# Optimization experiments

Hardware: AMD Instinct MI355X
Metric: run time of the kernel (lower is better)

The kernel has to match this reference:

```python
import jax, jax.numpy as jnp
import numpy as np

B, N, K, DIM = 8, 2048, 8, 128
EPS = 1e-5  # BatchNorm eps (torch default); BN evaluated in inference mode with running stats


def _xavier(key, o, i):
    lim = float(np.sqrt(6.0 / (i + o)))
    return jax.random.uniform(key, (o, i), jnp.float32, -lim, lim)


def setup_inputs() -> dict:
    key = jax.random.key(0)
    ks = jax.random.split(key, 8)
    x = jax.random.normal(ks[0], (B, 3, N), jnp.float32)
    w0 = _xavier(ks[1], DIM, 3)
    b0 = jnp.zeros((DIM,), jnp.float32)
    ws = jnp.stack([_xavier(ks[2 + i], DIM, DIM) for i in range(2)])  # [2,DIM,DIM]
    bs = jnp.zeros((2, DIM), jnp.float32)
    # BatchNorm (eval-mode) params / running stats, mildly randomized so math is exercised
    bn_g = 1.0 + 0.1 * jax.random.normal(ks[4], (3, DIM), jnp.float32)
    bn_b = 0.1 * jax.random.normal(ks[5], (3, DIM), jnp.float32)
    bn_m = 0.1 * jax.random.normal(ks[6], (3, DIM), jnp.float32)
    bn_v = jax.random.uniform(ks[7], (3, DIM), jnp.float32, 0.5, 1.5)
    return {"x": x, "w0": w0, "b0": b0, "ws": ws, "bs": bs,
            "bn_g": bn_g, "bn_b": bn_b, "bn_m": bn_m, "bn_v": bn_v}


def _group(x):
    # x: [B,3,N] -> relative kNN coords [B,3,N,K] (torch code uses [B,3,K,N]; axis order
    # is immaterial since the MLP is pointwise and the max is over the neighbor axis)
    inner = jnp.einsum('bcn,bcm->bnm', x, x)
    sq = jnp.sum(x * x, axis=1)                      # [B,N]
    dist = sq[:, :, None] - 2.0 * inner + sq[:, None, :]
    idx = jax.lax.top_k(-dist, K)[1]                 # [B,N,K] nearest (incl. self)
    grouped = jax.vmap(lambda xi, ii: xi[:, ii])(x, idx)  # [B,3,N,K]
    return grouped - x[:, :, :, None]


def _block(h, w, b, g, be, m, v):
    # 1x1 conv + eval-mode BatchNorm + ReLU over channel axis 1
    h = jnp.einsum('oc,bcnk->bonk', w, h) + b[None, :, None, None]
    scale = (g / jnp.sqrt(v + EPS))[None, :, None, None]
    h = (h - m[None, :, None, None]) * scale + be[None, :, None, None]
    return jax.nn.relu(h)


def reference(x, w0, b0, ws, bs, bn_g, bn_b, bn_m, bn_v):
    h = _group(x)                                    # [B,3,N,K]
    h = _block(h, w0, b0, bn_g[0], bn_b[0], bn_m[0], bn_v[0])
    for i in range(2):
        h = _block(h, ws[i], bs[i], bn_g[i + 1], bn_b[i + 1], bn_m[i + 1], bn_v[i + 1])
    return jnp.max(h, axis=3)                        # [B,DIM,N]
```

## Files before the change

kernel.cpp:

```cpp
#include <hip/hip_runtime.h>


#define EPSF 1e-5f
#define FMAXV 3.402823466e+38f

#define NB 8
#define NN 2048
#define KNBR 8
#define DIMF 128
#define NQ (NB * NN)
#define NPAIR (NQ * KNBR)

#define OFF16_W1H 0
#define OFF16_W1L 16384
#define OFF16_W2H 32768
#define OFF16_W2L 49152
#define OFF_C1 32896
#define OFF_C2 33024
#define OFF_W0F 33152
#define OFF_IDX 33792

typedef __attribute__((ext_vector_type(4))) float f32x4;
typedef __attribute__((ext_vector_type(8))) short short8v;

__device__ __forceinline__ float relu_f(float a) { return fmaxf(a, 0.0f); }

__device__ __forceinline__ void split3(float f, unsigned& hi, unsigned& lo) {
  const unsigned u = __float_as_uint(f);
  const unsigned h = (u + 0x7FFFu + ((u >> 16) & 1u)) >> 16;
  const float hf = __uint_as_float(h << 16);
  lo = __float_as_uint(f - hf) >> 16;
  hi = h;
}

__device__ __forceinline__ f32x4 mfma16x16x32bf(short8v a, short8v b, f32x4 c) {
  return __builtin_amdgcn_mfma_f32_16x16x32_bf16(a, b, c, 0, 0, 0);
}

#define KCSWAP(a, b)                  \
  {                                   \
    const float mn_ = fminf(a, b);    \
    const float mx_ = fmaxf(a, b);    \
    (a) = mn_; (b) = mx_;             \
  }

#define SORT8(d0, d1, d2, d3, d4, d5, d6, d7)                   \
  KCSWAP(d0, d1) KCSWAP(d2, d3) KCSWAP(d4, d5) KCSWAP(d6, d7)   \
  KCSWAP(d0, d2) KCSWAP(d1, d3) KCSWAP(d4, d6) KCSWAP(d5, d7)   \
  KCSWAP(d1, d2) KCSWAP(d5, d6)                                 \
  KCSWAP(d0, d4) KCSWAP(d1, d5) KCSWAP(d2, d6) KCSWAP(d3, d7)   \
  KCSWAP(d2, d4) KCSWAP(d3, d5)                                 \
  KCSWAP(d1, d2) KCSWAP(d3, d4) KCSWAP(d5, d6)

#define KCLEAN8()                                               \
  KCSWAP(k0, k4) KCSWAP(k1, k5) KCSWAP(k2, k6) KCSWAP(k3, k7)   \
  KCSWAP(k0, k2) KCSWAP(k1, k3) KCSWAP(k4, k6) KCSWAP(k5, k7)   \
  KCSWAP(k0, k1) KCSWAP(k2, k3) KCSWAP(k4, k5) KCSWAP(k6, k7)

#define KFOLD8(d0, d1, d2, d3, d4, d5, d6, d7)                  \
  {                                                             \
    k0 = fminf(k0, d7); k1 = fminf(k1, d6);                     \
    k2 = fminf(k2, d5); k3 = fminf(k3, d4);                     \
    k4 = fminf(k4, d3); k5 = fminf(k5, d2);                     \
    k6 = fminf(k6, d1); k7 = fminf(k7, d0);                     \
    KCLEAN8()                                                   \
  }

#define KMERGE(mv)                                              \
  {                                                             \
    const float q0_ = __shfl_xor(k0, mv, 64);                   \
    const float q1_ = __shfl_xor(k1, mv, 64);                   \
    const float q2_ = __shfl_xor(k2, mv, 64);                   \
    const float q3_ = __shfl_xor(k3, mv, 64);                   \
    const float q4_ = __shfl_xor(k4, mv, 64);                   \
    const float q5_ = __shfl_xor(k5, mv, 64);                   \
    const float q6_ = __shfl_xor(k6, mv, 64);                   \
    const float q7_ = __shfl_xor(k7, mv, 64);                   \
    k0 = fminf(k0, q7_); k1 = fminf(k1, q6_);                   \
    k2 = fminf(k2, q5_); k3 = fminf(k3, q4_);                   \
    k4 = fminf(k4, q3_); k5 = fminf(k5, q2_);                   \
    k6 = fminf(k6, q1_); k7 = fminf(k7, q0_);                   \
    KCLEAN8()                                                   \
  }

__global__ __launch_bounds__(512, 4) void knn_kernel(
    const float* __restrict__ x, const float* __restrict__ w0,
    const float* __restrict__ b0, const float* __restrict__ wstk,
    const float* __restrict__ bstk, const float* __restrict__ g,
    const float* __restrict__ be, const float* __restrict__ bm,
    const float* __restrict__ bv, float* __restrict__ ws) {
  __shared__ float2 xyp[2080];
  __shared__ float2 zsp[2080];
  const int t = threadIdx.x;
  const int bid = blockIdx.x;

  if (bid >= 1024) {
    const int i = (bid - 1024) * 512 + t;
    unsigned short* __restrict__ wsh = (unsigned short*)ws;
    const int fo = i >> 7, k = i & 127;
    const float s1 = g[128 + fo] / sqrtf(bv[128 + fo] + EPSF);
    const float s2 = g[256 + fo] / sqrtf(bv[256 + fo] + EPSF);
    unsigned h1, l1, h2, l2;
    split3(wstk[i] * s1, h1, l1);
    split3(wstk[16384 + i] * s2, h2, l2);
    const int dst = ((fo >> 4) * 4 + (k >> 5)) * 512 +
                    (((k >> 3) & 3) * 16 + (fo & 15)) * 8 + (k & 7);
    wsh[OFF16_W1H + dst] = (unsigned short)h1;
    wsh[OFF16_W1L + dst] = (unsigned short)l1;
    wsh[OFF16_W2H + dst] = (unsigned short)h2;
    wsh[OFF16_W2L + dst] = (unsigned short)l2;
    if (bid == 1024 && t < 128) {
      const int f = t;
      const float s0 = g[f] / sqrtf(bv[f] + EPSF);
      const float s1b = g[128 + f] / sqrtf(bv[128 + f] + EPSF);
      const float s2b = g[256 + f] / sqrtf(bv[256 + f] + EPSF);
      ws[OFF_C1 + f] = (bstk[f] - bm[128 + f]) * s1b + be[128 + f];
      ws[OFF_C2 + f] = (bstk[128 + f] - bm[256 + f]) * s2b + be[256 + f];
      float4 wv;
      wv.x = w0[3 * f + 0] * s0;
      wv.y = w0[3 * f + 1] * s0;
      wv.z = w0[3 * f + 2] * s0;
      wv.w = (b0[f] - bm[f]) * s0 + be[f];
      *((float4*)(ws + OFF_W0F) + f) = wv;
    }
    return;
  }

  const int bb = bid >> 7;
  const int qloc0 = (bid & 127) * 16;
  const float* __restrict__ xb = x + bb * 3 * NN;

#pragma unroll
  for (int k = 0; k < 4; ++k) {
    const int i = t + k * 512;
    const float a0 = xb[i];
    const float a1 = xb[2048 + i];
    const float a2 = xb[4096 + i];
    const float sq = fmaf(a2, a2, fmaf(a1, a1, a0 * a0));
    const int ii = i + (i >> 6);
    xyp[ii] = make_float2(a0, a1);
    zsp[ii] = make_float2(a2, sq);
  }

  const int qi = t >> 5;
  const int sg = t & 31;
  const int n = qloc0 + qi;
  const int q = bb * NN + n;
  const float qx0 = xb[n], qx1 = xb[2048 + n], qx2 = xb[4096 + n];
  const float sqn = fmaf(qx2, qx2, fmaf(qx1, qx1, qx0 * qx0));
  __syncthreads();

  const float2* __restrict__ xr = xyp + sg * 65;
  const float2* __restrict__ zr = zsp + sg * 65;

  float dv[64];
  float k0 = FMAXV, k1 = FMAXV, k2 = FMAXV, k3 = FMAXV,
        k4 = FMAXV, k5 = FMAXV, k6 = FMAXV, k7 = FMAXV;
#pragma unroll
  for (int bt = 0; bt < 8; ++bt) {
    float d0, d1, d2, d3, d4, d5, d6, d7;
#define KD(j, dj)                                                        \
    {                                                                    \
      const float2 cxy = xr[bt * 8 + (j)];                               \
      const float2 czs = zr[bt * 8 + (j)];                               \
      const float inner =                                                \
          fmaf(qx2, czs.x, fmaf(qx1, cxy.y, qx0 * cxy.x));               \
      dj = (sqn - 2.0f * inner) + czs.y;                                 \
    }
    KD(0, d0) KD(1, d1) KD(2, d2) KD(3, d3)
    KD(4, d4) KD(5, d5) KD(6, d6) KD(7, d7)
#undef KD
    dv[bt * 8 + 0] = d0; dv[bt * 8 + 1] = d1;
    dv[bt * 8 + 2] = d2; dv[bt * 8 + 3] = d3;
    dv[bt * 8 + 4] = d4; dv[bt * 8 + 5] = d5;
    dv[bt * 8 + 6] = d6; dv[bt * 8 + 7] = d7;
    SORT8(d0, d1, d2, d3, d4, d5, d6, d7)
    KFOLD8(d0, d1, d2, d3, d4, d5, d6, d7)
  }

  KMERGE(1) KMERGE(2) KMERGE(4) KMERGE(8) KMERGE(16)
  const float thr = k7;

  unsigned am = 0, bm2 = 0;
#pragma unroll
  for (int mm = 0; mm < 32; ++mm) am |= (dv[mm] <= thr) ? (1u << mm) : 0u;
#pragma unroll
  for (int mm = 0; mm < 32; ++mm)
    bm2 |= (dv[32 + mm] <= thr) ? (1u << mm) : 0u;

  const int cnt = __popc(am) + __popc(bm2);
  int inc = cnt, tq;
  tq = __shfl_up(inc, 1, 32); inc += (sg >= 1) ? tq : 0;
  tq = __shfl_up(inc, 2, 32); inc += (sg >= 2) ? tq : 0;
  tq = __shfl_up(inc, 4, 32); inc += (sg >= 4) ? tq : 0;
  tq = __shfl_up(inc, 8, 32); inc += (sg >= 8) ? tq : 0;
  tq = __shfl_up(inc, 16, 32); inc += (sg >= 16) ? tq : 0;
  int pos = inc - cnt;

  int* __restrict__ idxg = (int*)(ws + OFF_IDX);
  {
    unsigned w = am;
    while (w) {
      const int b = __ffs(w) - 1;
      w &= w - 1;
      if (pos < 8) idxg[q * 8 + pos] = bb * NN + sg * 64 + b;
      ++pos;
    }
    w = bm2;
    while (w) {
      const int b = __ffs(w) - 1;
      w &= w - 1;
      if (pos < 8) idxg[q * 8 + pos] = bb * NN + sg * 64 + 32 + b;
      ++pos;
    }
  }
}

__global__ __launch_bounds__(256, 2) void fused_kernel(
    const float* __restrict__ x, float* __restrict__ ws,
    float* __restrict__ out) {
  extern __shared__ char smem[];
  unsigned* __restrict__ H = (unsigned*)(smem + 32768);
  float* __restrict__ OS = (float*)(smem + 49152);
  float4* __restrict__ W0L = (float4*)(smem + 65536);

  const int* __restrict__ idxg = (const int*)(ws + OFF_IDX);
  const unsigned short* __restrict__ wsu = (const unsigned short*)ws;

  const int t = threadIdx.x;
  const int lane = t & 63, w = t >> 6;
  const int wc = w;
  const int bid = blockIdx.x;
  const int bb = bid & 7, qseg = bid >> 3;
  const int chunk0 = bb * 512 + qseg * 8;
  const float* __restrict__ xb = x + bb * 3 * NN;

  if (t < 128) {
    const float4 wv = *((const float4*)(ws + OFF_W0F) + t);
    W0L[((t & 7) << 4) | (t >> 3)] = wv;
  }

  short8v w1h[2][4], w1l[2][4], w2h[2][4], w2l[2][4];
#pragma unroll
  for (int ft = 0; ft < 2; ++ft)
#pragma unroll
    for (int ks = 0; ks < 4; ++ks) {
      const int off = ((wc * 2 + ft) * 4 + ks) * 512 + lane * 8;
      w1h[ft][ks] = *(const short8v*)(wsu + OFF16_W1H + off);
      w1l[ft][ks] = *(const short8v*)(wsu + OFF16_W1L + off);
      w2h[ft][ks] = *(const short8v*)(wsu + OFF16_W2H + off);
      w2l[ft][ks] = *(const short8v*)(wsu + OFF16_W2L + off);
    }

  const float c1v0 = (ws + OFF_C1)[wc * 32 + (lane & 15)];
  const float c1v1 = (ws + OFF_C1)[wc * 32 + 16 + (lane & 15)];
  const float c2v0 = (ws + OFF_C2)[wc * 32 + (lane & 15)];
  const float c2v1 = (ws + OFF_C2)[wc * 32 + 16 + (lane & 15)];

  const int row = t >> 3, part8 = t & 7;
  __syncthreads();

#define PACK_WRITE_A(base, hv, kc)                              \
  {                                                             \
    unsigned hh[8], ll[8];                                      \
    _Pragma("unroll") for (int e = 0; e < 8; ++e)               \
        split3(hv[e], hh[e], ll[e]);                            \
    int4 hp, lp;                                                \
    hp.x = (int)(hh[0] | (hh[1] << 16));                        \
    hp.y = (int)(hh[2] | (hh[3] << 16));                        \
    hp.z = (int)(hh[4] | (hh[5] << 16));                        \
    hp.w = (int)(hh[6] | (hh[7] << 16));                        \
    lp.x = (int)(ll[0] | (ll[1] << 16));                        \
    lp.y = (int)(ll[2] | (ll[3] << 16));                        \
    lp.z = (int)(ll[4] | (ll[5] << 16));                        \
    lp.w = (int)(ll[6] | (ll[7] << 16));                        \
    const int col = (kc) ^ (row & 7);                           \
    *(int4*)((base) + row * 256 + col * 16) = hp;               \
    *(int4*)((base) + 8192 + row * 256 + col * 16) = lp;        \
  }

#define STAGE_A(base, R0, R1, R2)                               \
  {                                                             \
    float hv0[8], hv1[8];                                       \
    _Pragma("unroll") for (int e = 0; e < 8; ++e) {             \
      const float4 wa = W0L[e * 16 + part8 * 2];                \
      const float4 wb = W0L[e * 16 + part8 * 2 + 1];            \
      hv0[e] = relu_f(                                          \
          fmaf(wa.z, R2, fmaf(wa.y, R1, fmaf(wa.x, R0, wa.w))));\
      hv1[e] = relu_f(                                          \
          fmaf(wb.z, R2, fmaf(wb.y, R1, fmaf(wb.x, R0, wb.w))));\
    }                                                           \
    PACK_WRITE_A(base, hv0, part8 * 2)                          \
    PACK_WRITE_A(base, hv1, part8 * 2 + 1)                      \
  }

  {
    const int gp = chunk0 * 32 + row;
    const int mg = idxg[gp];
    const int mloc = mg & 2047, nloc = (gp >> 3) & 2047;
    const float r0 = xb[mloc] - xb[nloc];
    const float r1 = xb[2048 + mloc] - xb[2048 + nloc];
    const float r2 = xb[4096 + mloc] - xb[4096 + nloc];
    STAGE_A(smem, r0, r1, r2)
  }
  __syncthreads();

#pragma unroll 1
  for (int j = 0; j < 8; ++j) {
    char* __restrict__ Acur = smem + (j & 1) * 16384;
    char* __restrict__ Anxt = smem + ((j & 1) ^ 1) * 16384;

    int mg_next = 0, gp_next = 0;
    if (j < 7) {
      gp_next = (chunk0 + j + 1) * 32 + row;
      mg_next = idxg[gp_next];
    }

    f32x4 acc[2][2];
#pragma unroll
    for (int pt = 0; pt < 2; ++pt)
#pragma unroll
      for (int ft = 0; ft < 2; ++ft) acc[pt][ft] = (f32x4){0.f, 0.f, 0.f, 0.f};
    __builtin_amdgcn_s_setprio(1);
#pragma unroll
    for (int ks = 0; ks < 4; ++ks) {
      const int kc = ks * 4 + (lane >> 4);
#pragma unroll
      for (int pt = 0; pt < 2; ++pt) {
        const int arow = pt * 16 + (lane & 15);
        const int col = kc ^ (arow & 7);
        const short8v ah = *(const short8v*)(Acur + arow * 256 + col * 16);
        const short8v al =
            *(const short8v*)(Acur + 8192 + arow * 256 + col * 16);
#pragma unroll
        for (int ft = 0; ft < 2; ++ft) {
          acc[pt][ft] = mfma16x16x32bf(al, w1h[ft][ks], acc[pt][ft]);
          acc[pt][ft] = mfma16x16x32bf(ah, w1l[ft][ks], acc[pt][ft]);
          acc[pt][ft] = mfma16x16x32bf(ah, w1h[ft][ks], acc[pt][ft]);
        }
      }
    }
    __builtin_amdgcn_s_setprio(0);

    float r0n = 0.f, r1n = 0.f, r2n = 0.f;
    if (j < 7) {
      const int mloc = mg_next & 2047, nloc = (gp_next >> 3) & 2047;
      r0n = xb[mloc] - xb[nloc];
      r1n = xb[2048 + mloc] - xb[2048 + nloc];
      r2n = xb[4096 + mloc] - xb[4096 + nloc];
    }

#pragma unroll
    for (int pt = 0; pt < 2; ++pt)
#pragma unroll
      for (int ft = 0; ft < 2; ++ft) {
        const int fo = wc * 32 + ft * 16 + (lane & 15);
        const int cc = fo >> 2;
        const float cb = ft ? c1v1 : c1v0;
#pragma unroll
        for (int reg = 0; reg < 4; ++reg) {
          const int p = pt * 16 + (lane >> 4) * 4 + reg;
          const float vv = relu_f(acc[pt][ft][reg] + cb);
          unsigned hh, ll;
          split3(vv, hh, ll);
          H[p * 128 + ((cc ^ (p & 7)) << 2) + (fo & 3)] = (hh << 16) | ll;
        }
      }
    __syncthreads();

    f32x4 acc2[2][2];
#pragma unroll
    for (int pt = 0; pt < 2; ++pt)
#pragma unroll
      for (int ft = 0; ft < 2; ++ft) acc2[pt][ft] = (f32x4){0.f, 0.f, 0.f, 0.f};
    __builtin_amdgcn_s_setprio(1);
#pragma unroll
    for (int ks = 0; ks < 4; ++ks) {
      const int cc0 = ks * 8 + (lane >> 4) * 2;
#pragma unroll
      for (int pt = 0; pt < 2; ++pt) {
        const int p = pt * 16 + (lane & 15);
        const int4 u0 = *(const int4*)&H[p * 128 + ((cc0 ^ (p & 7)) << 2)];
        const int4 u1 = *(const int4*)&H[p * 128 + (((cc0 + 1) ^ (p & 7)) << 2)];
        const unsigned uu[8] = {(unsigned)u0.x, (unsigned)u0.y, (unsigned)u0.z,
                                (unsigned)u0.w, (unsigned)u1.x, (unsigned)u1.y,
                                (unsigned)u1.z, (unsigned)u1.w};
        short8v ah, al;
#pragma unroll
        for (int e = 0; e < 8; ++e) {
          ah[e] = (short)(uu[e] >> 16);
          al[e] = (short)(uu[e] & 0xFFFFu);
        }
#pragma unroll
        for (int ft = 0; ft < 2; ++ft) {
          acc2[pt][ft] = mfma16x16x32bf(al, w2h[ft][ks], acc2[pt][ft]);
          acc2[pt][ft] = mfma16x16x32bf(ah, w2l[ft][ks], acc2[pt][ft]);
          acc2[pt][ft] = mfma16x16x32bf(ah, w2h[ft][ks], acc2[pt][ft]);
        }
      }
    }
    __builtin_amdgcn_s_setprio(0);
    __syncthreads();

    {
      const int g = lane >> 4;
#pragma unroll
      for (int pt = 0; pt < 2; ++pt)
#pragma unroll
        for (int ft = 0; ft < 2; ++ft) {
          const int fo = wc * 32 + ft * 16 + (lane & 15);
          const float cb = ft ? c2v1 : c2v0;
          const float v0 = relu_f(acc2[pt][ft][0] + cb);
          const float v1 = relu_f(acc2[pt][ft][1] + cb);
          const float v2 = relu_f(acc2[pt][ft][2] + cb);
          const float v3 = relu_f(acc2[pt][ft][3] + cb);
          float m = fmaxf(fmaxf(v0, v1), fmaxf(v2, v3));
          m = fmaxf(m, __shfl_xor(m, 16, 64));
          if ((g & 1) == 0) {
            const int qloc = pt * 2 + (g >> 1);
            OS[(j * 4 + qloc) * 128 + fo] = m;
          }
        }
    }

    if (j < 7) {
      STAGE_A(Anxt, r0n, r1n, r2n)
    }
    __syncthreads();
  }

  {
    const int f = t >> 1, seg = t & 1;
    float* __restrict__ op =
        out + (long)(bb * 128 + f) * 2048 + qseg * 32 + seg * 16;
#pragma unroll
    for (int u = 0; u < 4; ++u) {
      float4 o;
      o.x = OS[(seg * 16 + u * 4 + 0) * 128 + f];
      o.y = OS[(seg * 16 + u * 4 + 1) * 128 + f];
      o.z = OS[(seg * 16 + u * 4 + 2) * 128 + f];
      o.w = OS[(seg * 16 + u * 4 + 3) * 128 + f];
      *(float4*)(op + u * 4) = o;
    }
  }
}

extern "C" void kernel_launch(void* const* d_in, const int* in_sizes, int n_in,
                              void* d_out, int out_size, void* d_ws,
                              size_t ws_size, hipStream_t stream) {
  (void)in_sizes; (void)n_in; (void)out_size; (void)ws_size;
  const float* x = (const float*)d_in[0];
  const float* w0 = (const float*)d_in[1];
  const float* b0 = (const float*)d_in[2];
  const float* wst = (const float*)d_in[3];
  const float* bst = (const float*)d_in[4];
  const float* g = (const float*)d_in[5];
  const float* be = (const float*)d_in[6];
  const float* bm = (const float*)d_in[7];
  const float* bv = (const float*)d_in[8];
  float* out = (float*)d_out;
  float* ws = (float*)d_ws;

  hipFuncSetAttribute((const void*)fused_kernel,
                      hipFuncAttributeMaxDynamicSharedMemorySize, 69632);

  knn_kernel<<<1056, 512, 0, stream>>>(x, w0, b0, wst, bst, g, be, bm, bv, ws);
  fused_kernel<<<512, 256, 67584, stream>>>(x, ws, out);
}
```

Before: 60.90 us.

## Software-pipeline layer-1 and layer-2 GEMMs with double-buffered hidden tile

Restructures the fused MLP loop so the layer-2 GEMM of chunk j runs in the same phase as the layer-1 GEMM of chunk j+1, using a double-buffered hidden-activation tile in LDS. This cuts one block-wide barrier per iteration and lets the two MFMA streams interleave. The per-block output staging buffer is halved and flushed in two parts, and dynamic LDS grows, which could limit how many blocks fit per CU.

Result: faster. 59.28 us (median of 2 runs) (-2.7%).

```diff
diff --git a/kernel.cpp b/kernel.cpp
--- a/kernel.cpp
+++ b/kernel.cpp
@@ -220,9 +220,8 @@
     const float* __restrict__ x, float* __restrict__ ws,
     float* __restrict__ out) {
   extern __shared__ char smem[];
-  unsigned* __restrict__ H = (unsigned*)(smem + 32768);
-  float* __restrict__ OS = (float*)(smem + 49152);
-  float4* __restrict__ W0L = (float4*)(smem + 65536);
+  float* __restrict__ OS = (float*)(smem + 65536);
+  float4* __restrict__ W0L = (float4*)(smem + 73728);
 
   const int* __restrict__ idxg = (const int*)(ws + OFF_IDX);
   const unsigned short* __restrict__ wsu = (const unsigned short*)ws;
@@ -294,155 +293,159 @@
     PACK_WRITE_A(base, hv1, part8 * 2 + 1)                      \
   }
 
+#define G1_TO_H(Abase, Hbase)                                           \
+  {                                                                     \
+    f32x4 acc[2][2];                                                    \
+    _Pragma("unroll") for (int pt = 0; pt < 2; ++pt)                    \
+        _Pragma("unroll") for (int ft = 0; ft < 2; ++ft)                \
+            acc[pt][ft] = (f32x4){0.f, 0.f, 0.f, 0.f};                  \
+    __builtin_amdgcn_s_setprio(1);                                      \
+    _Pragma("unroll") for (int ks = 0; ks < 4; ++ks) {                  \
+      const int kc = ks * 4 + (lane >> 4);                              \
+      _Pragma("unroll") for (int pt = 0; pt < 2; ++pt) {                \
+        const int arow = pt * 16 + (lane & 15);                         \
+        const int col = kc ^ (arow & 7);                                \
+        const short8v ah =                                              \
+            *(const short8v*)((Abase) + arow * 256 + col * 16);         \
+        const short8v al =                                              \
+            *(const short8v*)((Abase) + 8192 + arow * 256 + col * 16);  \
+        _Pragma("unroll") for (int ft = 0; ft < 2; ++ft) {              \
+          acc[pt][ft] = mfma16x16x32bf(al, w1h[ft][ks], acc[pt][ft]);   \
+          acc[pt][ft] = mfma16x16x32bf(ah, w1l[ft][ks], acc[pt][ft]);   \
+          acc[pt][ft] = mfma16x16x32bf(ah, w1h[ft][ks], acc[pt][ft]);   \
+        }                                                               \
+      }                                                                 \
+    }                                                                   \
+    __builtin_amdgcn_s_setprio(0);                                      \
+    unsigned* __restrict__ Hp = (unsigned*)(Hbase);                     \
+    _Pragma("unroll") for (int pt = 0; pt < 2; ++pt)                    \
+        _Pragma("unroll") for (int ft = 0; ft < 2; ++ft) {              \
+      const int fo = wc * 32 + ft * 16 + (lane & 15);                   \
+      const int cc = fo >> 2;                                           \
+      const float cb = ft ? c1v1 : c1v0;                                \
+      _Pragma("unroll") for (int reg = 0; reg < 4; ++reg) {             \
+        const int p = pt * 16 + (lane >> 4) * 4 + reg;                  \
+        const float vv = relu_f(acc[pt][ft][reg] + cb);                 \
+        unsigned hh, ll;                                                \
+        split3(vv, hh, ll);                                             \
+        Hp[p * 128 + ((cc ^ (p & 7)) << 2) + (fo & 3)] = (hh << 16) | ll; \
+      }                                                                 \
+    }                                                                   \
+  }
+
+#define G2_TO_OS(Hbase, CH)                                             \
+  {                                                                     \
+    const unsigned* __restrict__ Hp = (const unsigned*)(Hbase);         \
+    f32x4 acc2[2][2];                                                   \
+    _Pragma("unroll") for (int pt = 0; pt < 2; ++pt)                    \
+        _Pragma("unroll") for (int ft = 0; ft < 2; ++ft)                \
+            acc2[pt][ft] = (f32x4){0.f, 0.f, 0.f, 0.f};                 \
+    __builtin_amdgcn_s_setprio(1);                                      \
+    _Pragma("unroll") for (int ks = 0; ks < 4; ++ks) {                  \
+      const int cc0 = ks * 8 + (lane >> 4) * 2;                         \
+      _Pragma("unroll") for (int pt = 0; pt < 2; ++pt) {                \
+        const int p = pt * 16 + (lane & 15);                            \
+        const int4 u0 = *(const int4*)&Hp[p * 128 + ((cc0 ^ (p & 7)) << 2)]; \
+        const int4 u1 =                                                 \
+            *(const int4*)&Hp[p * 128 + (((cc0 + 1) ^ (p & 7)) << 2)];  \
+        const unsigned uu[8] = {(unsigned)u0.x, (unsigned)u0.y,         \
+                                (unsigned)u0.z, (unsigned)u0.w,         \
+                                (unsigned)u1.x, (unsigned)u1.y,         \
+                                (unsigned)u1.z, (unsigned)u1.w};        \
+        short8v ah, al;                                                 \
+        _Pragma("unroll") for (int e = 0; e < 8; ++e) {                 \
+          ah[e] = (short)(uu[e] >> 16);                                 \
+          al[e] = (short)(uu[e] & 0xFFFFu);                             \
+        }                                                               \
+        _Pragma("unroll") for (int ft = 0; ft < 2; ++ft) {              \
+          acc2[pt][ft] = mfma16x16x32bf(al, w2h[ft][ks], acc2[pt][ft]); \
+          acc2[pt][ft] = mfma16x16x32bf(ah, w2l[ft][ks], acc2[pt][ft]); \
+          acc2[pt][ft] = mfma16x16x32bf(ah, w2h[ft][ks], acc2[pt][ft]); \
+        }                                                               \
+      }                                                                 \
+    }                                                                   \
+    __builtin_amdgcn_s_setprio(0);                                      \
+    const int g = lane >> 4;                                            \
+    _Pragma("unroll") for (int pt = 0; pt < 2; ++pt)                    \
+        _Pragma("unroll") for (int ft = 0; ft < 2; ++ft) {              \
+      const int fo = wc * 32 + ft * 16 + (lane & 15);                   \
+      const float cb = ft ? c2v1 : c2v0;                                \
+      const float v0 = relu_f(acc2[pt][ft][0] + cb);                    \
+      const float v1 = relu_f(acc2[pt][ft][1] + cb);                    \
+      const float v2 = relu_f(acc2[pt][ft][2] + cb);                    \
+      const float v3 = relu_f(acc2[pt][ft][3] + cb);                    \
+      float m = fmaxf(fmaxf(v0, v1), fmaxf(v2, v3));                    \
+      m = fmaxf(m, __shfl_xor(m, 16, 64));                              \
+      if ((g & 1) == 0) {                                               \
+        const int qloc = pt * 2 + (g >> 1);                             \
+        OS[(((CH) & 3) * 4 + qloc) * 128 + fo] = m;                     \
+      }                                                                 \
+    }                                                                   \
+  }
+
+#define OS_FLUSH(h)                                                     \
+  {                                                                     \
+    const int f = t >> 1, sh = t & 1;                                   \
+    float* __restrict__ op = out + (long)(bb * 128 + f) * 2048 +        \
+                             qseg * 32 + (h) * 16 + sh * 8;             \
+    float4 o1, o2;                                                      \
+    o1.x = OS[(sh * 8 + 0) * 128 + f];                                  \
+    o1.y = OS[(sh * 8 + 1) * 128 + f];                                  \
+    o1.z = OS[(sh * 8 + 2) * 128 + f];                                  \
+    o1.w = OS[(sh * 8 + 3) * 128 + f];                                  \
+    o2.x = OS[(sh * 8 + 4) * 128 + f];                                  \
+    o2.y = OS[(sh * 8 + 5) * 128 + f];                                  \
+    o2.z = OS[(sh * 8 + 6) * 128 + f];                                  \
+    o2.w = OS[(sh * 8 + 7) * 128 + f];                                  \
+    *(float4*)op = o1;                                                  \
+    *(float4*)(op + 4) = o2;                                            \
+  }
+
+#define LOAD_R(CH, MG, R0, R1, R2)                     \
+  {                                                    \
+    const int mloc = (MG) & 2047;                      \
+    const int nloc = ((((CH) * 32 + row)) >> 3) & 2047;\
+    R0 = xb[mloc] - xb[nloc];                          \
+    R1 = xb[2048 + mloc] - xb[2048 + nloc];            \
+    R2 = xb[4096 + mloc] - xb[4096 + nloc];            \
+  }
+
   {
-    const int gp = chunk0 * 32 + row;
-    const int mg = idxg[gp];
-    const int mloc = mg & 2047, nloc = (gp >> 3) & 2047;
-    const float r0 = xb[mloc] - xb[nloc];
-    const float r1 = xb[2048 + mloc] - xb[2048 + nloc];
-    const float r2 = xb[4096 + mloc] - xb[4096 + nloc];
+    const int mg0 = idxg[(chunk0 + 0) * 32 + row];
+    const int mg1 = idxg[(chunk0 + 1) * 32 + row];
+    float r0, r1, r2;
+    LOAD_R(chunk0 + 0, mg0, r0, r1, r2)
     STAGE_A(smem, r0, r1, r2)
-  }
-  __syncthreads();
+    __syncthreads();
+    G1_TO_H(smem, smem + 32768)
+    LOAD_R(chunk0 + 1, mg1, r0, r1, r2)
+    STAGE_A(smem + 16384, r0, r1, r2)
+    __syncthreads();
+  }
 
 #pragma unroll 1
   for (int j = 0; j < 8; ++j) {
-    char* __restrict__ Acur = smem + (j & 1) * 16384;
-    char* __restrict__ Anxt = smem + ((j & 1) ^ 1) * 16384;
-
-    int mg_next = 0, gp_next = 0;
+    int mg2 = 0;
+    if (j < 6) mg2 = idxg[(chunk0 + j + 2) * 32 + row];
+
+    G2_TO_OS(smem + 32768 + (j & 1) * 16384, j)
+
     if (j < 7) {
-      gp_next = (chunk0 + j + 1) * 32 + row;
-      mg_next = idxg[gp_next];
-    }
-
-    f32x4 acc[2][2];
-#pragma unroll
-    for (int pt = 0; pt < 2; ++pt)
-#pragma unroll
-      for (int ft = 0; ft < 2; ++ft) acc[pt][ft] = (f32x4){0.f, 0.f, 0.f, 0.f};
-    __builtin_amdgcn_s_setprio(1);
-#pragma unroll
-    for (int ks = 0; ks < 4; ++ks) {
-      const int kc = ks * 4 + (lane >> 4);
-#pragma unroll
-      for (int pt = 0; pt < 2; ++pt) {
-        const int arow = pt * 16 + (lane & 15);
-        const int col = kc ^ (arow & 7);
-        const short8v ah = *(const short8v*)(Acur + arow * 256 + col * 16);
-        const short8v al =
-            *(const short8v*)(Acur + 8192 + arow * 256 + col * 16);
-#pragma unroll
-        for (int ft = 0; ft < 2; ++ft) {
-          acc[pt][ft] = mfma16x16x32bf(al, w1h[ft][ks], acc[pt][ft]);
-          acc[pt][ft] = mfma16x16x32bf(ah, w1l[ft][ks], acc[pt][ft]);
-          acc[pt][ft] = mfma16x16x32bf(ah, w1h[ft][ks], acc[pt][ft]);
-        }
+      G1_TO_H(smem + ((j + 1) & 1) * 16384,
+              smem + 32768 + ((j + 1) & 1) * 16384)
+      if (j < 6) {
+        float r0, r1, r2;
+        LOAD_R(chunk0 + j + 2, mg2, r0, r1, r2)
+        STAGE_A(smem + (j & 1) * 16384, r0, r1, r2)
       }
     }
-    __builtin_amdgcn_s_setprio(0);
-
-    float r0n = 0.f, r1n = 0.f, r2n = 0.f;
-    if (j < 7) {
-      const int mloc = mg_next & 2047, nloc = (gp_next >> 3) & 2047;
-      r0n = xb[mloc] - xb[nloc];
-      r1n = xb[2048 + mloc] - xb[2048 + nloc];
-      r2n = xb[4096 + mloc] - xb[4096 + nloc];
-    }
-
-#pragma unroll
-    for (int pt = 0; pt < 2; ++pt)
-#pragma unroll
-      for (int ft = 0; ft < 2; ++ft) {
-        const int fo = wc * 32 + ft * 16 + (lane & 15);
-        const int cc = fo >> 2;
-        const float cb = ft ? c1v1 : c1v0;
-#pragma unroll
-        for (int reg = 0; reg < 4; ++reg) {
-          const int p = pt * 16 + (lane >> 4) * 4 + reg;
-          const float vv = relu_f(acc[pt][ft][reg] + cb);
-          unsigned hh, ll;
-          split3(vv, hh, ll);
-          H[p * 128 + ((cc ^ (p & 7)) << 2) + (fo & 3)] = (hh << 16) | ll;
-        }
-      }
     __syncthreads();
-
-    f32x4 acc2[2][2];
-#pragma unroll
-    for (int pt = 0; pt < 2; ++pt)
-#pragma unroll
-      for (int ft = 0; ft < 2; ++ft) acc2[pt][ft] = (f32x4){0.f, 0.f, 0.f, 0.f};
-    __builtin_amdgcn_s_setprio(1);
-#pragma unroll
-    for (int ks = 0; ks < 4; ++ks) {
-      const int cc0 = ks * 8 + (lane >> 4) * 2;
-#pragma unroll
-      for (int pt = 0; pt < 2; ++pt) {
-        const int p = pt * 16 + (lane & 15);
-        const int4 u0 = *(const int4*)&H[p * 128 + ((cc0 ^ (p & 7)) << 2)];
-        const int4 u1 = *(const int4*)&H[p * 128 + (((cc0 + 1) ^ (p & 7)) << 2)];
-        const unsigned uu[8] = {(unsigned)u0.x, (unsigned)u0.y, (unsigned)u0.z,
-                                (unsigned)u0.w, (unsigned)u1.x, (unsigned)u1.y,
-                                (unsigned)u1.z, (unsigned)u1.w};
-        short8v ah, al;
-#pragma unroll
-        for (int e = 0; e < 8; ++e) {
-          ah[e] = (short)(uu[e] >> 16);
-          al[e] = (short)(uu[e] & 0xFFFFu);
-        }
-#pragma unroll
-        for (int ft = 0; ft < 2; ++ft) {
-          acc2[pt][ft] = mfma16x16x32bf(al, w2h[ft][ks], acc2[pt][ft]);
-          acc2[pt][ft] = mfma16x16x32bf(ah, w2l[ft][ks], acc2[pt][ft]);
-          acc2[pt][ft] = mfma16x16x32bf(ah, w2h[ft][ks], acc2[pt][ft]);
-        }
-      }
-    }
-    __builtin_amdgcn_s_setprio(0);
-    __syncthreads();
-
-    {
-      const int g = lane >> 4;
-#pragma unroll
-      for (int pt = 0; pt < 2; ++pt)
-#pragma unroll
-        for (int ft = 0; ft < 2; ++ft) {
-          const int fo = wc * 32 + ft * 16 + (lane & 15);
-          const float cb = ft ? c2v1 : c2v0;
-          const float v0 = relu_f(acc2[pt][ft][0] + cb);
-          const float v1 = relu_f(acc2[pt][ft][1] + cb);
-          const float v2 = relu_f(acc2[pt][ft][2] + cb);
-          const float v3 = relu_f(acc2[pt][ft][3] + cb);
-          float m = fmaxf(fmaxf(v0, v1), fmaxf(v2, v3));
-          m = fmaxf(m, __shfl_xor(m, 16, 64));
-          if ((g & 1) == 0) {
-            const int qloc = pt * 2 + (g >> 1);
-            OS[(j * 4 + qloc) * 128 + fo] = m;
-          }
-        }
-    }
-
-    if (j < 7) {
-      STAGE_A(Anxt, r0n, r1n, r2n)
-    }
-    __syncthreads();
-  }
-
-  {
-    const int f = t >> 1, seg = t & 1;
-    float* __restrict__ op =
-        out + (long)(bb * 128 + f) * 2048 + qseg * 32 + seg * 16;
-#pragma unroll
-    for (int u = 0; u < 4; ++u) {
-      float4 o;
-      o.x = OS[(seg * 16 + u * 4 + 0) * 128 + f];
-      o.y = OS[(seg * 16 + u * 4 + 1) * 128 + f];
-      o.z = OS[(seg * 16 + u * 4 + 2) * 128 + f];
-      o.w = OS[(seg * 16 + u * 4 + 3) * 128 + f];
-      *(float4*)(op + u * 4) = o;
-    }
-  }
+    if (j == 3) {
+      OS_FLUSH(0)
+      __syncthreads();
+    }
+  }
+  OS_FLUSH(1)
 }
 
 extern "C" void kernel_launch(void* const* d_in, const int* in_sizes, int n_in,
@@ -462,8 +465,8 @@
   float* ws = (float*)d_ws;
 
   hipFuncSetAttribute((const void*)fused_kernel,
-                      hipFuncAttributeMaxDynamicSharedMemorySize, 69632);
+                      hipFuncAttributeMaxDynamicSharedMemorySize, 75776);
 
   knn_kernel<<<1056, 512, 0, stream>>>(x, w0, b0, wst, bst, g, be, bm, bv, ws);
-  fused_kernel<<<512, 256, 67584, stream>>>(x, ws, out);
+  fused_kernel<<<512, 256, 75776, stream>>>(x, ws, out);
 }
```
